# Optimization experiments

Hardware: AMD Instinct MI355X
Metric: run time of the kernel (lower is better)

Reference implementation:

```python
import jax, jax.numpy as jnp
import numpy as np

INPUT_DIM = 16
LW = 128          # layerwidth
NB_LAYERS = 4
NB_X = 4096
NB_THETA = 128
PARAM_COUNT = INPUT_DIM * LW + LW + (NB_LAYERS - 1) * (LW * LW + LW) + LW + 1  # 51841


def setup_inputs() -> dict:
    k1, k2 = jax.random.split(jax.random.key(0))
    x = jax.random.normal(k1, (NB_X, INPUT_DIM), dtype=jnp.float32)
    theta = jax.random.normal(k2, (NB_THETA, PARAM_COUNT), dtype=jnp.float32)
    return {"x": x, "theta": theta}


def reference(x, theta):
    # x: [nb_x, input_dim], theta: [nb_theta, param_count]
    t = theta.shape[0]
    off = 0
    # first layer: W0 [t, LW, INPUT_DIM], b0 [t, LW]
    W0 = theta[:, off:off + INPUT_DIM * LW].reshape(t, LW, INPUT_DIM); off += INPUT_DIM * LW
    b0 = theta[:, off:off + LW]; off += LW
    h = jnp.tanh(jnp.einsum('thi,xi->txh', W0, x) + b0[:, None, :])  # [t, nb_x, LW]
    # hidden layers
    for _ in range(NB_LAYERS - 1):
        W = theta[:, off:off + LW * LW].reshape(t, LW, LW); off += LW * LW
        b = theta[:, off:off + LW]; off += LW
        h = jnp.tanh(jnp.einsum('tho,txo->txh', W, h) + b[:, None, :])
    # output layer: Wl [t, LW], bl [t, 1]
    Wl = theta[:, off:off + LW]; off += LW
    bl = theta[:, off:off + 1]
    out = jnp.einsum('th,txh->tx', Wl, h)[..., None] + bl[:, None, :]  # [t, nb_x, 1]
    return out
```

## Files before the change

kernel.cpp:

```cpp
#include <hip/hip_runtime.h>


#define IND      16
#define LWD      128
#define THREADS  256
#define PARAMS   51841

#define WS_L0    12582912
#define WS_X     (WS_L0 + 128 * 8192)
#define WS_TOTAL (WS_X + 32 * 8192)

#define LDS_B    32768
#define LDS_WL   (32768 + 1536)
#define LDS_SZ   (32768 + 1536 + 520)

typedef _Float16 f16x8 __attribute__((ext_vector_type(8)));
typedef _Float16 f16x4 __attribute__((ext_vector_type(4)));
typedef float    f32x16 __attribute__((ext_vector_type(16)));
typedef float    f32x4v __attribute__((ext_vector_type(4)));
typedef unsigned u32x2  __attribute__((ext_vector_type(2)));

union U4 { unsigned u[4]; f16x8 v; };

__device__ __forceinline__ float fast_tanh(float v) {
    float e = __builtin_amdgcn_exp2f(v * 2.8853900817779268f);
    return 1.0f - 2.0f * __builtin_amdgcn_rcpf(e + 1.0f);
}
__device__ __forceinline__ unsigned pkf16(float a, float b) {
    unsigned short ua = __builtin_bit_cast(unsigned short, (_Float16)a);
    unsigned short ub = __builtin_bit_cast(unsigned short, (_Float16)b);
    return (unsigned)ua | ((unsigned)ub << 16);
}
#define MFMA(A, B, C) __builtin_amdgcn_mfma_f32_32x32x16_f16((A), (B), (C), 0, 0, 0)

__device__ __forceinline__ void gload16(const void* g, void* l) {
    __builtin_amdgcn_global_load_lds(
        (const __attribute__((address_space(1))) void*)g,
        (__attribute__((address_space(3))) void*)l, 16, 0, 0);
}

__device__ __forceinline__ void conv8(const float* __restrict__ s, char* hidst, char* lodst) {
    float v[8];
    *reinterpret_cast<float4*>(v)     = *reinterpret_cast<const float4*>(s);
    *reinterpret_cast<float4*>(v + 4) = *reinterpret_cast<const float4*>(s + 4);
    f16x8 hi, lo;
#pragma unroll
    for (int i = 0; i < 8; ++i) {
        hi[i] = (_Float16)v[i];
        lo[i] = (_Float16)(v[i] - (float)hi[i]);
    }
    *reinterpret_cast<f16x8*>(hidst) = hi;
    *reinterpret_cast<f16x8*>(lodst) = lo;
}

__global__ __launch_bounds__(256)
void prep_kernel(const float* __restrict__ theta, const float* __restrict__ xin,
                 char* __restrict__ ws)
{
    const int b = blockIdx.x, tid = threadIdx.x;
    if (b < 3072) {
        const int t = b / 24, rem = b % 24, li = rem >> 3, hblk = rem & 7;
        const int h  = hblk * 16 + (tid >> 4);
        const int kc = (tid >> 1) & 7, kh = tid & 1;
        const float* src = theta + (size_t)t * PARAMS + 2176 + li * 16512
                         + h * 128 + kc * 16 + kh * 8;
        float v[8];
        *reinterpret_cast<float4*>(v)     = *reinterpret_cast<const float4*>(src);
        *reinterpret_cast<float4*>(v + 4) = *reinterpret_cast<const float4*>(src + 4);
        f16x8 p;
#pragma unroll
        for (int i = 0; i < 8; ++i) p[i] = (_Float16)v[i];
        char* img = ws + ((size_t)(t * 3 + li) << 15);
        *reinterpret_cast<f16x8*>(img + ((h >> 5) * 8 + kc) * 1024
                                      + (kh * 32 + (h & 31)) * 16) = p;
    } else if (b < 3136) {
        const int gid = (b - 3072) * 256 + tid;
        const int t = gid >> 7, h = gid & 127;
        const float* src = theta + (size_t)t * PARAMS + h * IND;
        char* dst = ws + WS_L0 + (size_t)t * 8192 + h * 32;
        conv8(src,     dst,      dst + 4096);
        conv8(src + 8, dst + 16, dst + 4096 + 16);
    } else {
        const int row = (b - 3136) * 256 + tid;
        const float* src = xin + (size_t)row * IND;
        char* dst = ws + WS_X + (size_t)(row >> 7) * 8192 + (row & 127) * 32;
        conv8(src,     dst,      dst + 4096);
        conv8(src + 8, dst + 16, dst + 4096 + 16);
    }
}

__global__ __launch_bounds__(THREADS, 4)
void mlp_main(const float* __restrict__ theta, const char* __restrict__ ws,
              float* __restrict__ out)
{
    __shared__ __align__(16) char sL[LDS_SZ];

    const int tid = threadIdx.x, bid = blockIdx.x;
    const int sw  = (bid & 7) * 512 + (bid >> 3);
    const int t   = sw >> 5, xt = sw & 31;
    const float* __restrict__ th = theta + (size_t)t * PARAMS;
    const int lane = tid & 63, w = tid >> 6, r31 = lane & 31, khalf = lane >> 5;
    const int bpa  = (lane ^ 32) << 2;

    {
        const char* img = ws + ((size_t)(t * 3) << 15);
#pragma unroll
        for (int c = 0; c < 8; ++c)
            gload16(img + (w + c * 4) * 1024 + lane * 16, sL + (w + c * 4) * 1024);
    }
    for (int k = tid; k < 513; k += THREADS) {
        float v = (k < 384) ? th[2176 + (k >> 7) * 16512 + 16384 + (k & 127)]
                            : th[51712 + (k - 384)];
        *reinterpret_cast<float*>(sL + LDS_B + k * 4) = v;
    }

    f32x16 acc[4];
    {
        const char* w0i = ws + WS_L0 + (size_t)t  * 8192;
        const char* xi  = ws + WS_X  + (size_t)xt * 8192;
        const int ro = r31 * 32 + khalf * 16;
        const f16x8 B0h = *reinterpret_cast<const f16x8*>(xi + w * 1024 + ro);
        const f16x8 B0l = *reinterpret_cast<const f16x8*>(xi + 4096 + w * 1024 + ro);
#pragma unroll
        for (int tt = 0; tt < 4; ++tt) {
#pragma unroll
            for (int g = 0; g < 4; ++g) {
                const float4 bv = *reinterpret_cast<const float4*>(
                    th + 2048 + tt * 32 + g * 8 + khalf * 4);
                acc[tt][4 * g + 0] = bv.x; acc[tt][4 * g + 1] = bv.y;
                acc[tt][4 * g + 2] = bv.z; acc[tt][4 * g + 3] = bv.w;
            }
            const f16x8 Ah = *reinterpret_cast<const f16x8*>(w0i + tt * 1024 + ro);
            const f16x8 Al = *reinterpret_cast<const f16x8*>(w0i + 4096 + tt * 1024 + ro);
            acc[tt] = MFMA(Al, B0h, acc[tt]);
            acc[tt] = MFMA(Ah, B0l, acc[tt]);
            acc[tt] = MFMA(Ah, B0h, acc[tt]);
        }
    }

    f16x8 Bf[8];
    auto activate_pack = [&]() {
#pragma unroll
        for (int tt = 0; tt < 4; ++tt) {
            unsigned P0[4], P1[4];
#pragma unroll
            for (int g = 0; g < 4; ++g) {
                const float v0 = fast_tanh(acc[tt][4 * g + 0]);
                const float v1 = fast_tanh(acc[tt][4 * g + 1]);
                const float v2 = fast_tanh(acc[tt][4 * g + 2]);
                const float v3 = fast_tanh(acc[tt][4 * g + 3]);
                P0[g] = pkf16(v0, v1);
                P1[g] = pkf16(v2, v3);
            }
#pragma unroll
            for (int j = 0; j < 2; ++j) {
#if __has_builtin(__builtin_amdgcn_permlane32_swap)
                const u32x2 r0 = __builtin_amdgcn_permlane32_swap(
                    P0[2 * j], P0[2 * j + 1], false, false);
                const u32x2 r1 = __builtin_amdgcn_permlane32_swap(
                    P1[2 * j], P1[2 * j + 1], false, false);
                U4 u;
                u.u[0] = r0[0]; u.u[1] = r1[0]; u.u[2] = r0[1]; u.u[3] = r1[1];
#else
                const unsigned s0 = khalf ? P0[2 * j] : P0[2 * j + 1];
                const unsigned s1 = khalf ? P1[2 * j] : P1[2 * j + 1];
                const unsigned q0 = (unsigned)__builtin_amdgcn_ds_bpermute(bpa, (int)s0);
                const unsigned q1 = (unsigned)__builtin_amdgcn_ds_bpermute(bpa, (int)s1);
                U4 u;
                u.u[0] = khalf ? q0 : P0[2 * j];
                u.u[1] = khalf ? q1 : P1[2 * j];
                u.u[2] = khalf ? P0[2 * j + 1] : q0;
                u.u[3] = khalf ? P1[2 * j + 1] : q1;
#endif
                Bf[2 * tt + j] = u.v;
            }
        }
    };
    activate_pack();
    __syncthreads();

#pragma unroll
    for (int l = 1; l <= 3; ++l) {
        __builtin_amdgcn_s_setprio(1);
#pragma unroll
        for (int tt = 0; tt < 4; ++tt) {
#pragma unroll
            for (int g = 0; g < 4; ++g) {
                const f32x4v bv = *reinterpret_cast<const f32x4v*>(
                    sL + LDS_B + (l - 1) * 512 + (tt * 32 + g * 8) * 4 + khalf * 16);
                acc[tt][4 * g + 0] = bv[0]; acc[tt][4 * g + 1] = bv[1];
                acc[tt][4 * g + 2] = bv[2]; acc[tt][4 * g + 3] = bv[3];
            }
#pragma unroll
            for (int kc = 0; kc < 8; ++kc) {
                const f16x8 a = *reinterpret_cast<const f16x8*>(
                    sL + (tt * 8 + kc) * 1024 + lane * 16);
                acc[tt] = MFMA(a, Bf[kc], acc[tt]);
            }
        }
        __builtin_amdgcn_s_setprio(0);
        if (l < 3) {
            __syncthreads();
            const char* img = ws + ((size_t)(t * 3 + l) << 15);
#pragma unroll
            for (int c = 0; c < 8; ++c)
                gload16(img + (w + c * 4) * 1024 + lane * 16, sL + (w + c * 4) * 1024);
            activate_pack();
            __syncthreads();
        }
    }

    float s = 0.0f;
#pragma unroll
    for (int tt = 0; tt < 4; ++tt)
#pragma unroll
        for (int g = 0; g < 4; ++g) {
            const f32x4v wv = *reinterpret_cast<const f32x4v*>(
                sL + LDS_WL + (tt * 32 + g * 8) * 4 + khalf * 16);
#pragma unroll
            for (int q = 0; q < 4; ++q)
                s = fmaf(fast_tanh(acc[tt][4 * g + q]), wv[q], s);
        }
    const float sp = __builtin_bit_cast(float,
        __builtin_amdgcn_ds_bpermute(bpa, __builtin_bit_cast(int, s)));
    const float res = s + sp + *reinterpret_cast<const float*>(sL + LDS_WL + 512);
    if (!khalf) out[(size_t)t * 4096 + xt * 128 + w * 32 + r31] = res;
}

__global__ __launch_bounds__(THREADS, 1)
void mlp_kernel_fb(const float* __restrict__ xin,
                   const float* __restrict__ theta,
                   float* __restrict__ out)
{
    __shared__ __align__(16) _Float16 sH   [128 * LWD];
    __shared__ __align__(16) _Float16 sWhi [LWD * LWD];
    __shared__ __align__(16) _Float16 sWlo [LWD * LWD];
    __shared__ __align__(16) _Float16 sX0hi[128 * IND];
    __shared__ __align__(16) _Float16 sX0lo[128 * IND];
    __shared__ __align__(16) _Float16 sW0hi[LWD * IND];
    __shared__ __align__(16) _Float16 sW0lo[LWD * IND];
    __shared__ float sB[2][LWD];
    __shared__ float sWl[LWD + 1];

    const int tid = threadIdx.x;
    const int bid = blockIdx.x;
    const int sw  = (bid & 7) * 512 + (bid >> 3);
    const int t   = sw >> 5;
    const int xt  = sw & 31;
    const float* __restrict__ th = theta + (size_t)t * PARAMS;
    const float* __restrict__ xg = xin   + (size_t)xt * (128 * IND);

#pragma unroll
    for (int j = 0; j < 2; ++j) {
        const int flat = j * 1024 + tid * 4;
        const float4 v = *reinterpret_cast<const float4*>(xg + flat);
        _Float16 h0 = (_Float16)v.x, h1 = (_Float16)v.y, h2 = (_Float16)v.z, h3 = (_Float16)v.w;
        f16x4 ph = {h0, h1, h2, h3};
        f16x4 pl = {(_Float16)(v.x - (float)h0), (_Float16)(v.y - (float)h1),
                    (_Float16)(v.z - (float)h2), (_Float16)(v.w - (float)h3)};
        *reinterpret_cast<f16x4*>(&sX0hi[flat]) = ph;
        *reinterpret_cast<f16x4*>(&sX0lo[flat]) = pl;
    }
#pragma unroll
    for (int j = 0; j < 2; ++j) {
        const int flat = j * 1024 + tid * 4;
        const float a0 = th[flat], a1 = th[flat + 1], a2 = th[flat + 2], a3 = th[flat + 3];
        _Float16 h0 = (_Float16)a0, h1 = (_Float16)a1, h2 = (_Float16)a2, h3 = (_Float16)a3;
        f16x4 ph = {h0, h1, h2, h3};
        f16x4 pl = {(_Float16)(a0 - (float)h0), (_Float16)(a1 - (float)h1),
                    (_Float16)(a2 - (float)h2), (_Float16)(a3 - (float)h3)};
        *reinterpret_cast<f16x4*>(&sW0hi[flat]) = ph;
        *reinterpret_cast<f16x4*>(&sW0lo[flat]) = pl;
    }
    if (tid < LWD) sB[0][tid] = th[IND * LWD + tid];
    __syncthreads();

    const int lane  = tid & 63;
    const int w     = tid >> 6;
    const int r31   = lane & 31;
    const int khalf = lane >> 5;
    const int hb    = (w >> 1) * 64;
    const int xb    = (w & 1) * 64;
    const int hA0 = hb + r31,  hA1 = hb + 32 + r31;
    const int xB0 = xb + r31,  xB1 = xb + 32 + r31;
    const int swzA0 = (hA0 & 15) << 4, swzA1 = (hA1 & 15) << 4;
    const int swzB0 = (xB0 & 15) << 4, swzB1 = (xB1 & 15) << 4;

    f32x16 acc[2][2];

    {
        const int kb = khalf * 16;
        f16x8 ah[2], al[2], bh[2], bl[2];
        ah[0] = *reinterpret_cast<const f16x8*>((const char*)sW0hi + hA0 * 32 + kb);
        ah[1] = *reinterpret_cast<const f16x8*>((const char*)sW0hi + hA1 * 32 + kb);
        al[0] = *reinterpret_cast<const f16x8*>((const char*)sW0lo + hA0 * 32 + kb);
        al[1] = *reinterpret_cast<const f16x8*>((const char*)sW0lo + hA1 * 32 + kb);
        bh[0] = *reinterpret_cast<const f16x8*>((const char*)sX0hi + xB0 * 32 + kb);
        bh[1] = *reinterpret_cast<const f16x8*>((const char*)sX0hi + xB1 * 32 + kb);
        bl[0] = *reinterpret_cast<const f16x8*>((const char*)sX0lo + xB0 * 32 + kb);
        bl[1] = *reinterpret_cast<const f16x8*>((const char*)sX0lo + xB1 * 32 + kb);
#pragma unroll
        for (int tt = 0; tt < 2; ++tt)
#pragma unroll
            for (int tx = 0; tx < 2; ++tx) {
                f32x16 a;
#pragma unroll
                for (int i = 0; i < 16; ++i) a[i] = 0.0f;
                a = MFMA(al[tt], bh[tx], a);
                a = MFMA(ah[tt], bl[tx], a);
                a = MFMA(ah[tt], bh[tx], a);
                acc[tt][tx] = a;
            }
    }

    auto epilogue = [&](const float* __restrict__ bb) {
#pragma unroll
        for (int tt = 0; tt < 2; ++tt)
#pragma unroll
            for (int tx = 0; tx < 2; ++tx) {
                const int xw  = xb + tx * 32 + r31;
                const int swz = (xw & 15) << 4;
#pragma unroll
                for (int g = 0; g < 4; ++g) {
                    const int hbase = hb + tt * 32 + g * 8 + khalf * 4;
                    f16x4 pk;
#pragma unroll
                    for (int q = 0; q < 4; ++q) {
                        const float v = acc[tt][tx][g * 4 + q] + bb[hbase + q];
                        pk[q] = (_Float16)(1.0f - 2.0f * __builtin_amdgcn_rcpf(
                            __builtin_amdgcn_exp2f(v * 2.8853900817779268f) + 1.0f));
                    }
                    *reinterpret_cast<f16x4*>((char*)sH + xw * 256 + ((hbase * 2) ^ swz)) = pk;
                }
            }
    };

    for (int l = 0; l < 3; ++l) {
        __syncthreads();
        const float* __restrict__ wsrc = th + 2176 + l * 16512;
#pragma unroll
        for (int j = 0; j < 16; ++j) {
            const int flat = j * 1024 + tid * 4;
            const int hrow = flat >> 7;
            const int o    = flat & 127;
            const float a0 = wsrc[flat], a1 = wsrc[flat + 1], a2 = wsrc[flat + 2], a3 = wsrc[flat + 3];
            _Float16 h0 = (_Float16)a0, h1 = (_Float16)a1, h2 = (_Float16)a2, h3 = (_Float16)a3;
            f16x4 ph = {h0, h1, h2, h3};
            f16x4 pl = {(_Float16)(a0 - (float)h0), (_Float16)(a1 - (float)h1),
                        (_Float16)(a2 - (float)h2), (_Float16)(a3 - (float)h3)};
            const int boff = hrow * 256 + ((o * 2) ^ ((hrow & 15) << 4));
            *reinterpret_cast<f16x4*>((char*)sWhi + boff) = ph;
            *reinterpret_cast<f16x4*>((char*)sWlo + boff) = pl;
        }
        if (tid < LWD) sB[(l + 1) & 1][tid] = wsrc[LWD * LWD + tid];
        if (l == 2) {
            if (tid < LWD) sWl[tid] = th[51712 + tid];
            if (tid == LWD) sWl[LWD] = th[51840];
        }

        epilogue(sB[l & 1]);
        __syncthreads();

#pragma unroll
        for (int tt = 0; tt < 2; ++tt)
#pragma unroll
            for (int tx = 0; tx < 2; ++tx)
#pragma unroll
                for (int i = 0; i < 16; ++i) acc[tt][tx][i] = 0.0f;
#pragma unroll
        for (int kc = 0; kc < 8; ++kc) {
            const int kb = kc * 32 + khalf * 16;
            f16x8 ah[2], al[2], bv[2];
            ah[0] = *reinterpret_cast<const f16x8*>((const char*)sWhi + hA0 * 256 + (kb ^ swzA0));
            ah[1] = *reinterpret_cast<const f16x8*>((const char*)sWhi + hA1 * 256 + (kb ^ swzA1));
            al[0] = *reinterpret_cast<const f16x8*>((const char*)sWlo + hA0 * 256 + (kb ^ swzA0));
            al[1] = *reinterpret_cast<const f16x8*>((const char*)sWlo + hA1 * 256 + (kb ^ swzA1));
            bv[0] = *reinterpret_cast<const f16x8*>((const char*)sH   + xB0 * 256 + (kb ^ swzB0));
            bv[1] = *reinterpret_cast<const f16x8*>((const char*)sH   + xB1 * 256 + (kb ^ swzB1));
#pragma unroll
            for (int tt = 0; tt < 2; ++tt)
#pragma unroll
                for (int tx = 0; tx < 2; ++tx) {
                    acc[tt][tx] = MFMA(al[tt], bv[tx], acc[tt][tx]);
                    acc[tt][tx] = MFMA(ah[tt], bv[tx], acc[tt][tx]);
                }
        }
    }

    __syncthreads();
    epilogue(sB[1]);
    __syncthreads();

    if (tid < 128) {
        const int r   = tid;
        const int swz = (r & 15) << 4;
        float s = 0.0f;
#pragma unroll
        for (int c = 0; c < 16; ++c) {
            const int hc = (c + r) & 15;
            const f16x8 hv = *reinterpret_cast<const f16x8*>(
                (const char*)sH + r * 256 + ((hc * 16) ^ swz));
#pragma unroll
            for (int q = 0; q < 8; ++q) s += (float)hv[q] * sWl[hc * 8 + q];
        }
        out[(size_t)t * 4096 + (size_t)xt * 128 + r] = s + sWl[LWD];
    }
}

extern "C" void kernel_launch(void* const* d_in, const int* in_sizes, int n_in,
                              void* d_out, int out_size, void* d_ws, size_t ws_size,
                              hipStream_t stream)
{
    const float* x     = (const float*)d_in[0];
    const float* theta = (const float*)d_in[1];
    float* out = (float*)d_out;

    if (ws_size >= (size_t)WS_TOTAL) {
        prep_kernel<<<dim3(3152), dim3(256), 0, stream>>>(theta, x, (char*)d_ws);
        mlp_main<<<dim3(4096), dim3(THREADS), 0, stream>>>(theta, (const char*)d_ws, out);
    } else {
        mlp_kernel_fb<<<dim3(4096), dim3(THREADS), 0, stream>>>(x, theta, out);
    }
}
```

Baseline: 105.2 us.

## Fold biases and output layer into MFMA via ones-column trick

```diff
diff --git a/kernel.cpp b/kernel.cpp
--- a/kernel.cpp
+++ b/kernel.cpp
@@ -6,22 +6,28 @@
 #define THREADS  256
 #define PARAMS   51841
 
-#define WS_L0    12582912
-#define WS_X     (WS_L0 + 128 * 8192)
-#define WS_TOTAL (WS_X + 32 * 8192)
-
-#define LDS_B    32768
-#define LDS_WL   (32768 + 1536)
-#define LDS_SZ   (32768 + 1536 + 520)
+#define HID_STRIDE 36864
+#define WS_W0    (128 * 3 * HID_STRIDE)
+#define WS_XI    (WS_W0 + 128 * 16384)
+#define WS_TOTAL (WS_XI + 32 * 8192)
+
+#define LDS_WL   36864
+#define LDS_BL   37376
+#define LDS_SZ   37380
 
 typedef _Float16 f16x8 __attribute__((ext_vector_type(8)));
 typedef _Float16 f16x4 __attribute__((ext_vector_type(4)));
 typedef float    f32x16 __attribute__((ext_vector_type(16)));
-typedef float    f32x4v __attribute__((ext_vector_type(4)));
 typedef unsigned u32x2  __attribute__((ext_vector_type(2)));
 
 union U4 { unsigned u[4]; f16x8 v; };
 
+__device__ __forceinline__ f32x16 zero16() {
+    f32x16 z;
+#pragma unroll
+    for (int i = 0; i < 16; ++i) z[i] = 0.0f;
+    return z;
+}
 __device__ __forceinline__ float fast_tanh(float v) {
     float e = __builtin_amdgcn_exp2f(v * 2.8853900817779268f);
     return 1.0f - 2.0f * __builtin_amdgcn_rcpf(e + 1.0f);
@@ -70,20 +76,58 @@
         f16x8 p;
 #pragma unroll
         for (int i = 0; i < 8; ++i) p[i] = (_Float16)v[i];
-        char* img = ws + ((size_t)(t * 3 + li) << 15);
-        *reinterpret_cast<f16x8*>(img + ((h >> 5) * 8 + kc) * 1024
+        char* img = ws + (size_t)(t * 3 + li) * HID_STRIDE;
+        *reinterpret_cast<f16x8*>(img + ((h >> 5) * 9 + kc) * 1024
                                       + (kh * 32 + (h & 31)) * 16) = p;
-    } else if (b < 3136) {
-        const int gid = (b - 3072) * 256 + tid;
+    } else if (b < 3456) {
+        const int idx = b - 3072, t = idx / 3, li = idx % 3;
+        const int tt = tid >> 6, l6 = tid & 63, kh = l6 >> 5, row = l6 & 31;
+        f16x8 p;
+#pragma unroll
+        for (int i = 0; i < 8; ++i) p[i] = (_Float16)0.0f;
+        if (kh == 0) {
+            const float bv = theta[(size_t)t * PARAMS + 2176 + li * 16512
+                                   + 16384 + tt * 32 + row];
+            p[0] = (_Float16)bv;
+            p[1] = (_Float16)(bv - (float)p[0]);
+        }
+        char* img = ws + (size_t)(t * 3 + li) * HID_STRIDE;
+        *reinterpret_cast<f16x8*>(img + (tt * 9 + 8) * 1024 + l6 * 16) = p;
+    } else if (b < 3520) {
+        const int gid = (b - 3456) * 256 + tid;
         const int t = gid >> 7, h = gid & 127;
         const float* src = theta + (size_t)t * PARAMS + h * IND;
-        char* dst = ws + WS_L0 + (size_t)t * 8192 + h * 32;
+        char* dst = ws + WS_W0 + (size_t)t * 16384 + h * 32;
         conv8(src,     dst,      dst + 4096);
         conv8(src + 8, dst + 16, dst + 4096 + 16);
+    } else if (b < 3648) {
+        const int t = b - 3520;
+        const float* th = theta + (size_t)t * PARAMS;
+        char* base = ws + WS_W0 + (size_t)t * 16384;
+        {
+            const int tt = tid >> 6, l6 = tid & 63, kh = l6 >> 5, row = l6 & 31;
+            f16x8 p;
+#pragma unroll
+            for (int i = 0; i < 8; ++i) p[i] = (_Float16)0.0f;
+            if (kh == 0) {
+                const float bv = th[2048 + tt * 32 + row];
+                p[0] = (_Float16)bv;
+                p[1] = (_Float16)(bv - (float)p[0]);
+            }
+            *reinterpret_cast<f16x8*>(base + 8192 + tt * 1024 + l6 * 16) = p;
+        }
+        if (tid < 32) {
+            const int kc = tid >> 1, kh = tid & 1;
+            const float* src = th + 51712 + kc * 16 + kh * 8;
+            f16x8 p;
+#pragma unroll
+            for (int i = 0; i < 8; ++i) p[i] = (_Float16)src[i];
+            *reinterpret_cast<f16x8*>(base + 12288 + tid * 16) = p;
+        }
     } else {
-        const int row = (b - 3136) * 256 + tid;
+        const int row = (b - 3648) * 256 + tid;
         const float* src = xin + (size_t)row * IND;
-        char* dst = ws + WS_X + (size_t)(row >> 7) * 8192 + (row & 127) * 32;
+        char* dst = ws + WS_XI + (size_t)(row >> 7) * 8192 + (row & 127) * 32;
         conv8(src,     dst,      dst + 4096);
         conv8(src + 8, dst + 16, dst + 4096 + 16);
     }
@@ -101,40 +145,42 @@
     const float* __restrict__ th = theta + (size_t)t * PARAMS;
     const int lane = tid & 63, w = tid >> 6, r31 = lane & 31, khalf = lane >> 5;
     const int bpa  = (lane ^ 32) << 2;
+    (void)bpa;
+
+    U4 ubias;
+    ubias.u[0] = khalf ? 0u : 0x3C003C00u;
+    ubias.u[1] = 0u; ubias.u[2] = 0u; ubias.u[3] = 0u;
+    const f16x8 Bones = ubias.v;
 
     {
-        const char* img = ws + ((size_t)(t * 3) << 15);
-#pragma unroll
-        for (int c = 0; c < 8; ++c)
-            gload16(img + (w + c * 4) * 1024 + lane * 16, sL + (w + c * 4) * 1024);
-    }
-    for (int k = tid; k < 513; k += THREADS) {
-        float v = (k < 384) ? th[2176 + (k >> 7) * 16512 + 16384 + (k & 127)]
-                            : th[51712 + (k - 384)];
-        *reinterpret_cast<float*>(sL + LDS_B + k * 4) = v;
+        const char* img = ws + (size_t)(t * 3) * HID_STRIDE;
+#pragma unroll
+        for (int c = 0; c < 9; ++c)
+            gload16(img + (c * 4 + w) * 1024 + lane * 16, sL + (c * 4 + w) * 1024);
+        if (tid < 32)
+            gload16(ws + WS_W0 + (size_t)t * 16384 + 12288 + tid * 16,
+                    sL + LDS_WL + tid * 16);
+        if (tid == 32) *reinterpret_cast<float*>(sL + LDS_BL) = th[51840];
     }
 
     f32x16 acc[4];
     {
-        const char* w0i = ws + WS_L0 + (size_t)t  * 8192;
-        const char* xi  = ws + WS_X  + (size_t)xt * 8192;
+        const char* w0i = ws + WS_W0 + (size_t)t  * 16384;
+        const char* xi  = ws + WS_XI + (size_t)xt * 8192;
         const int ro = r31 * 32 + khalf * 16;
         const f16x8 B0h = *reinterpret_cast<const f16x8*>(xi + w * 1024 + ro);
         const f16x8 B0l = *reinterpret_cast<const f16x8*>(xi + 4096 + w * 1024 + ro);
 #pragma unroll
         for (int tt = 0; tt < 4; ++tt) {
-#pragma unroll
-            for (int g = 0; g < 4; ++g) {
-                const float4 bv = *reinterpret_cast<const float4*>(
-                    th + 2048 + tt * 32 + g * 8 + khalf * 4);
-                acc[tt][4 * g + 0] = bv.x; acc[tt][4 * g + 1] = bv.y;
-                acc[tt][4 * g + 2] = bv.z; acc[tt][4 * g + 3] = bv.w;
-            }
+            f32x16 a = zero16();
+            const f16x8 Ab = *reinterpret_cast<const f16x8*>(w0i + 8192 + tt * 1024 + lane * 16);
+            a = MFMA(Ab, Bones, a);
             const f16x8 Ah = *reinterpret_cast<const f16x8*>(w0i + tt * 1024 + ro);
             const f16x8 Al = *reinterpret_cast<const f16x8*>(w0i + 4096 + tt * 1024 + ro);
-            acc[tt] = MFMA(Al, B0h, acc[tt]);
-            acc[tt] = MFMA(Ah, B0l, acc[tt]);
-            acc[tt] = MFMA(Ah, B0h, acc[tt]);
+            a = MFMA(Al, B0h, a);
+            a = MFMA(Ah, B0l, a);
+            a = MFMA(Ah, B0h, a);
+            acc[tt] = a;
         }
     }
 
@@ -184,47 +230,39 @@
         __builtin_amdgcn_s_setprio(1);
 #pragma unroll
         for (int tt = 0; tt < 4; ++tt) {
-#pragma unroll
-            for (int g = 0; g < 4; ++g) {
-                const f32x4v bv = *reinterpret_cast<const f32x4v*>(
-                    sL + LDS_B + (l - 1) * 512 + (tt * 32 + g * 8) * 4 + khalf * 16);
-                acc[tt][4 * g + 0] = bv[0]; acc[tt][4 * g + 1] = bv[1];
-                acc[tt][4 * g + 2] = bv[2]; acc[tt][4 * g + 3] = bv[3];
-            }
+            f32x16 a = zero16();
+            a = MFMA(*reinterpret_cast<const f16x8*>(
+                         sL + (tt * 9 + 8) * 1024 + lane * 16), Bones, a);
 #pragma unroll
             for (int kc = 0; kc < 8; ++kc) {
-                const f16x8 a = *reinterpret_cast<const f16x8*>(
-                    sL + (tt * 8 + kc) * 1024 + lane * 16);
-                acc[tt] = MFMA(a, Bf[kc], acc[tt]);
-            }
+                const f16x8 av = *reinterpret_cast<const f16x8*>(
+                    sL + (tt * 9 + kc) * 1024 + lane * 16);
+                a = MFMA(av, Bf[kc], a);
+            }
+            acc[tt] = a;
         }
         __builtin_amdgcn_s_setprio(0);
         if (l < 3) {
             __syncthreads();
-            const char* img = ws + ((size_t)(t * 3 + l) << 15);
-#pragma unroll
-            for (int c = 0; c < 8; ++c)
-                gload16(img + (w + c * 4) * 1024 + lane * 16, sL + (w + c * 4) * 1024);
+            const char* img = ws + (size_t)(t * 3 + l) * HID_STRIDE;
+#pragma unroll
+            for (int c = 0; c < 9; ++c)
+                gload16(img + (c * 4 + w) * 1024 + lane * 16, sL + (c * 4 + w) * 1024);
             activate_pack();
             __syncthreads();
         }
     }
 
-    float s = 0.0f;
-#pragma unroll
-    for (int tt = 0; tt < 4; ++tt)
-#pragma unroll
-        for (int g = 0; g < 4; ++g) {
-            const f32x4v wv = *reinterpret_cast<const f32x4v*>(
-                sL + LDS_WL + (tt * 32 + g * 8) * 4 + khalf * 16);
-#pragma unroll
-            for (int q = 0; q < 4; ++q)
-                s = fmaf(fast_tanh(acc[tt][4 * g + q]), wv[q], s);
-        }
-    const float sp = __builtin_bit_cast(float,
-        __builtin_amdgcn_ds_bpermute(bpa, __builtin_bit_cast(int, s)));
-    const float res = s + sp + *reinterpret_cast<const float*>(sL + LDS_WL + 512);
-    if (!khalf) out[(size_t)t * 4096 + xt * 128 + w * 32 + r31] = res;
+    activate_pack();
+    const float bl = *reinterpret_cast<const float*>(sL + LDS_BL);
+    f32x16 af = zero16();
+#pragma unroll
+    for (int kc = 0; kc < 8; ++kc) {
+        const f16x8 wv = *reinterpret_cast<const f16x8*>(
+            sL + LDS_WL + (kc * 2 + khalf) * 16);
+        af = MFMA(wv, Bf[kc], af);
+    }
+    if (!khalf) out[(size_t)t * 4096 + xt * 128 + w * 32 + r31] = af[0] + bl;
 }
 
 __global__ __launch_bounds__(THREADS, 1)
@@ -416,7 +454,7 @@
     float* out = (float*)d_out;
 
     if (ws_size >= (size_t)WS_TOTAL) {
-        prep_kernel<<<dim3(3152), dim3(256), 0, stream>>>(theta, x, (char*)d_ws);
+        prep_kernel<<<dim3(3664), dim3(256), 0, stream>>>(theta, x, (char*)d_ws);
         mlp_main<<<dim3(4096), dim3(THREADS), 0, stream>>>(theta, (const char*)d_ws, out);
     } else {
         mlp_kernel_fb<<<dim3(4096), dim3(THREADS), 0, stream>>>(x, theta, out);
```

Result: slower. 109.6 us (+4.2%).

## Drop LDS staging, prescale weights by tanh constant, read weights directly from global

Applied to the files above, without the earlier changes.

```diff
diff --git a/kernel.cpp b/kernel.cpp
--- a/kernel.cpp
+++ b/kernel.cpp
@@ -2,17 +2,15 @@
 
 
 #define IND      16
-#define LWD      128
 #define THREADS  256
 #define PARAMS   51841
-
-#define WS_L0    12582912
-#define WS_X     (WS_L0 + 128 * 8192)
-#define WS_TOTAL (WS_X + 32 * 8192)
-
-#define LDS_B    32768
-#define LDS_WL   (32768 + 1536)
-#define LDS_SZ   (32768 + 1536 + 520)
+#define SCALE    2.8853900817779268f
+
+#define HID_STRIDE 32768
+#define WS_T     (128 * 3 * HID_STRIDE)
+#define T_STRIDE 16384
+#define WS_XI    (WS_T + 128 * T_STRIDE)
+#define WS_TOTAL (WS_XI + 32 * 8192)
 
 typedef _Float16 f16x8 __attribute__((ext_vector_type(8)));
 typedef _Float16 f16x4 __attribute__((ext_vector_type(4)));
@@ -22,32 +20,34 @@
 
 union U4 { unsigned u[4]; f16x8 v; };
 
-__device__ __forceinline__ float fast_tanh(float v) {
-    float e = __builtin_amdgcn_exp2f(v * 2.8853900817779268f);
-    return 1.0f - 2.0f * __builtin_amdgcn_rcpf(e + 1.0f);
-}
-__device__ __forceinline__ unsigned pkf16(float a, float b) {
-    unsigned short ua = __builtin_bit_cast(unsigned short, (_Float16)a);
-    unsigned short ub = __builtin_bit_cast(unsigned short, (_Float16)b);
-    return (unsigned)ua | ((unsigned)ub << 16);
-}
+__device__ __forceinline__ unsigned tanh2pk(float z0, float z1) {
+    const float t0 = __builtin_amdgcn_exp2f(-__builtin_fabsf(z0));
+    const float t1 = __builtin_amdgcn_exp2f(-__builtin_fabsf(z1));
+    const float d0 = t0 + 1.0f, d1 = t1 + 1.0f;
+    float r0 = __builtin_fmaf(d0, __builtin_fmaf(d0, 0.32302f, -1.45380f), 2.12094f);
+    float r1 = __builtin_fmaf(d1, __builtin_fmaf(d1, 0.32302f, -1.45380f), 2.12094f);
+    r0 = __builtin_fmaf(r0, __builtin_fmaf(-d0, r0, 1.0f), r0);
+    r1 = __builtin_fmaf(r1, __builtin_fmaf(-d1, r1, 1.0f), r1);
+    const float u0 = __builtin_fmaf(t0 * r0, -2.0f, 1.0f);
+    const float u1 = __builtin_fmaf(t1 * r1, -2.0f, 1.0f);
+    const float y0 = __builtin_copysignf(u0, z0);
+    const float y1 = __builtin_copysignf(u1, z1);
+    return __builtin_bit_cast(unsigned, __builtin_amdgcn_cvt_pkrtz(y0, y1));
+}
+
 #define MFMA(A, B, C) __builtin_amdgcn_mfma_f32_32x32x16_f16((A), (B), (C), 0, 0, 0)
 
-__device__ __forceinline__ void gload16(const void* g, void* l) {
-    __builtin_amdgcn_global_load_lds(
-        (const __attribute__((address_space(1))) void*)g,
-        (__attribute__((address_space(3))) void*)l, 16, 0, 0);
-}
-
-__device__ __forceinline__ void conv8(const float* __restrict__ s, char* hidst, char* lodst) {
+__device__ __forceinline__ void conv8(const float* __restrict__ s, char* hidst,
+                                      char* lodst, float scale) {
     float v[8];
     *reinterpret_cast<float4*>(v)     = *reinterpret_cast<const float4*>(s);
     *reinterpret_cast<float4*>(v + 4) = *reinterpret_cast<const float4*>(s + 4);
     f16x8 hi, lo;
 #pragma unroll
     for (int i = 0; i < 8; ++i) {
-        hi[i] = (_Float16)v[i];
-        lo[i] = (_Float16)(v[i] - (float)hi[i]);
+        const float sv = v[i] * scale;
+        hi[i] = (_Float16)sv;
+        lo[i] = (_Float16)(sv - (float)hi[i]);
     }
     *reinterpret_cast<f16x8*>(hidst) = hi;
     *reinterpret_cast<f16x8*>(lodst) = lo;
@@ -69,55 +69,56 @@
         *reinterpret_cast<float4*>(v + 4) = *reinterpret_cast<const float4*>(src + 4);
         f16x8 p;
 #pragma unroll
-        for (int i = 0; i < 8; ++i) p[i] = (_Float16)v[i];
-        char* img = ws + ((size_t)(t * 3 + li) << 15);
+        for (int i = 0; i < 8; ++i) p[i] = (_Float16)(v[i] * SCALE);
+        char* img = ws + (size_t)(t * 3 + li) * HID_STRIDE;
         *reinterpret_cast<f16x8*>(img + ((h >> 5) * 8 + kc) * 1024
                                       + (kh * 32 + (h & 31)) * 16) = p;
     } else if (b < 3136) {
         const int gid = (b - 3072) * 256 + tid;
         const int t = gid >> 7, h = gid & 127;
         const float* src = theta + (size_t)t * PARAMS + h * IND;
-        char* dst = ws + WS_L0 + (size_t)t * 8192 + h * 32;
-        conv8(src,     dst,      dst + 4096);
-        conv8(src + 8, dst + 16, dst + 4096 + 16);
+        char* dst = ws + WS_T + (size_t)t * T_STRIDE + h * 32;
+        conv8(src,     dst,      dst + 4096,      SCALE);
+        conv8(src + 8, dst + 16, dst + 4096 + 16, SCALE);
+    } else if (b < 3264) {
+        const int t = b - 3136;
+        const float* th = theta + (size_t)t * PARAMS;
+        char* base = ws + WS_T + (size_t)t * T_STRIDE;
+        if (tid < 128)
+            *reinterpret_cast<float*>(base + 8192 + tid * 4) = SCALE * th[2048 + tid];
+        for (int k = tid; k < 384; k += 256)
+            *reinterpret_cast<float*>(base + 8704 + k * 4) =
+                SCALE * th[2176 + (k >> 7) * 16512 + 16384 + (k & 127)];
+        if (tid < 128)
+            *reinterpret_cast<float*>(base + 10240 + tid * 4) = th[51712 + tid];
+        if (tid == 0)
+            *reinterpret_cast<float*>(base + 10752) = th[51840];
     } else {
-        const int row = (b - 3136) * 256 + tid;
+        const int row = (b - 3264) * 256 + tid;
         const float* src = xin + (size_t)row * IND;
-        char* dst = ws + WS_X + (size_t)(row >> 7) * 8192 + (row & 127) * 32;
-        conv8(src,     dst,      dst + 4096);
-        conv8(src + 8, dst + 16, dst + 4096 + 16);
-    }
-}
-
-__global__ __launch_bounds__(THREADS, 4)
-void mlp_main(const float* __restrict__ theta, const char* __restrict__ ws,
-              float* __restrict__ out)
+        char* dst = ws + WS_XI + (size_t)(row >> 7) * 8192 + (row & 127) * 32;
+        conv8(src,     dst,      dst + 4096,      1.0f);
+        conv8(src + 8, dst + 16, dst + 4096 + 16, 1.0f);
+    }
+}
+
+__global__ __launch_bounds__(THREADS, 3)
+void mlp_main(const char* __restrict__ ws, float* __restrict__ out)
 {
-    __shared__ __align__(16) char sL[LDS_SZ];
-
     const int tid = threadIdx.x, bid = blockIdx.x;
     const int sw  = (bid & 7) * 512 + (bid >> 3);
     const int t   = sw >> 5, xt = sw & 31;
-    const float* __restrict__ th = theta + (size_t)t * PARAMS;
     const int lane = tid & 63, w = tid >> 6, r31 = lane & 31, khalf = lane >> 5;
     const int bpa  = (lane ^ 32) << 2;
+    (void)bpa;
+
+    const char* wt = ws + WS_T + (size_t)t * T_STRIDE;
+
+    f32x16 acc[4];
+    f16x8  Bf[8];
 
     {
-        const char* img = ws + ((size_t)(t * 3) << 15);
-#pragma unroll
-        for (int c = 0; c < 8; ++c)
-            gload16(img + (w + c * 4) * 1024 + lane * 16, sL + (w + c * 4) * 1024);
-    }
-    for (int k = tid; k < 513; k += THREADS) {
-        float v = (k < 384) ? th[2176 + (k >> 7) * 16512 + 16384 + (k & 127)]
-                            : th[51712 + (k - 384)];
-        *reinterpret_cast<float*>(sL + LDS_B + k * 4) = v;
-    }
-
-    f32x16 acc[4];
-    {
-        const char* w0i = ws + WS_L0 + (size_t)t  * 8192;
-        const char* xi  = ws + WS_X  + (size_t)xt * 8192;
+        const char* xi = ws + WS_XI + (size_t)xt * 8192;
         const int ro = r31 * 32 + khalf * 16;
         const f16x8 B0h = *reinterpret_cast<const f16x8*>(xi + w * 1024 + ro);
         const f16x8 B0l = *reinterpret_cast<const f16x8*>(xi + 4096 + w * 1024 + ro);
@@ -125,32 +126,27 @@
         for (int tt = 0; tt < 4; ++tt) {
 #pragma unroll
             for (int g = 0; g < 4; ++g) {
-                const float4 bv = *reinterpret_cast<const float4*>(
-                    th + 2048 + tt * 32 + g * 8 + khalf * 4);
-                acc[tt][4 * g + 0] = bv.x; acc[tt][4 * g + 1] = bv.y;
-                acc[tt][4 * g + 2] = bv.z; acc[tt][4 * g + 3] = bv.w;
-            }
-            const f16x8 Ah = *reinterpret_cast<const f16x8*>(w0i + tt * 1024 + ro);
-            const f16x8 Al = *reinterpret_cast<const f16x8*>(w0i + 4096 + tt * 1024 + ro);
+                const f32x4v bv = *reinterpret_cast<const f32x4v*>(
+                    wt + 8192 + (tt * 32 + g * 8 + khalf * 4) * 4);
+                acc[tt][4 * g + 0] = bv[0]; acc[tt][4 * g + 1] = bv[1];
+                acc[tt][4 * g + 2] = bv[2]; acc[tt][4 * g + 3] = bv[3];
+            }
+            const f16x8 Ah = *reinterpret_cast<const f16x8*>(wt + tt * 1024 + ro);
+            const f16x8 Al = *reinterpret_cast<const f16x8*>(wt + 4096 + tt * 1024 + ro);
             acc[tt] = MFMA(Al, B0h, acc[tt]);
             acc[tt] = MFMA(Ah, B0l, acc[tt]);
             acc[tt] = MFMA(Ah, B0h, acc[tt]);
         }
     }
 
-    f16x8 Bf[8];
     auto activate_pack = [&]() {
 #pragma unroll
         for (int tt = 0; tt < 4; ++tt) {
             unsigned P0[4], P1[4];
 #pragma unroll
             for (int g = 0; g < 4; ++g) {
-                const float v0 = fast_tanh(acc[tt][4 * g + 0]);
-                const float v1 = fast_tanh(acc[tt][4 * g + 1]);
-                const float v2 = fast_tanh(acc[tt][4 * g + 2]);
-                const float v3 = fast_tanh(acc[tt][4 * g + 3]);
-                P0[g] = pkf16(v0, v1);
-                P1[g] = pkf16(v2, v3);
+                P0[g] = tanh2pk(acc[tt][4 * g + 0], acc[tt][4 * g + 1]);
+                P1[g] = tanh2pk(acc[tt][4 * g + 2], acc[tt][4 * g + 3]);
             }
 #pragma unroll
             for (int j = 0; j < 2; ++j) {
@@ -177,53 +173,68 @@
         }
     };
     activate_pack();
-    __syncthreads();
-
-#pragma unroll
-    for (int l = 1; l <= 3; ++l) {
-        __builtin_amdgcn_s_setprio(1);
+
+#pragma unroll
+    for (int l = 0; l < 3; ++l) {
+        const char* img  = ws + (size_t)(t * 3 + l) * HID_STRIDE;
+        const char* bias = wt + 8704 + l * 512;
 #pragma unroll
         for (int tt = 0; tt < 4; ++tt) {
 #pragma unroll
             for (int g = 0; g < 4; ++g) {
                 const f32x4v bv = *reinterpret_cast<const f32x4v*>(
-                    sL + LDS_B + (l - 1) * 512 + (tt * 32 + g * 8) * 4 + khalf * 16);
+                    bias + (tt * 32 + g * 8 + khalf * 4) * 4);
                 acc[tt][4 * g + 0] = bv[0]; acc[tt][4 * g + 1] = bv[1];
                 acc[tt][4 * g + 2] = bv[2]; acc[tt][4 * g + 3] = bv[3];
             }
-#pragma unroll
-            for (int kc = 0; kc < 8; ++kc) {
-                const f16x8 a = *reinterpret_cast<const f16x8*>(
-                    sL + (tt * 8 + kc) * 1024 + lane * 16);
-                acc[tt] = MFMA(a, Bf[kc], acc[tt]);
-            }
-        }
-        __builtin_amdgcn_s_setprio(0);
-        if (l < 3) {
-            __syncthreads();
-            const char* img = ws + ((size_t)(t * 3 + l) << 15);
-#pragma unroll
-            for (int c = 0; c < 8; ++c)
-                gload16(img + (w + c * 4) * 1024 + lane * 16, sL + (w + c * 4) * 1024);
-            activate_pack();
-            __syncthreads();
-        }
+        }
+#pragma unroll
+        for (int kc = 0; kc < 8; ++kc)
+#pragma unroll
+            for (int tt = 0; tt < 4; ++tt) {
+                const f16x8 av = *reinterpret_cast<const f16x8*>(
+                    img + (tt * 8 + kc) * 1024 + lane * 16);
+                acc[tt] = MFMA(av, Bf[kc], acc[tt]);
+            }
+        activate_pack();
     }
 
     float s = 0.0f;
 #pragma unroll
-    for (int tt = 0; tt < 4; ++tt)
-#pragma unroll
-        for (int g = 0; g < 4; ++g) {
-            const f32x4v wv = *reinterpret_cast<const f32x4v*>(
-                sL + LDS_WL + (tt * 32 + g * 8) * 4 + khalf * 16);
-#pragma unroll
-            for (int q = 0; q < 4; ++q)
-                s = fmaf(fast_tanh(acc[tt][4 * g + q]), wv[q], s);
-        }
+    for (int kc = 0; kc < 8; ++kc) {
+        (void)kc;
+    }
+    {
+        const char* wl = wt + 10240;
+#pragma unroll
+        for (int tt = 0; tt < 4; ++tt)
+#pragma unroll
+            for (int g = 0; g < 4; ++g) {
+                const f32x4v wv = *reinterpret_cast<const f32x4v*>(
+                    wl + (tt * 32 + g * 8 + khalf * 4) * 4);
+                const float z0 = acc[tt][4 * g + 0], z1 = acc[tt][4 * g + 1];
+                const float z2 = acc[tt][4 * g + 2], z3 = acc[tt][4 * g + 3];
+                const float e0 = __builtin_amdgcn_exp2f(-__builtin_fabsf(z0));
+                const float e1 = __builtin_amdgcn_exp2f(-__builtin_fabsf(z1));
+                const float e2 = __builtin_amdgcn_exp2f(-__builtin_fabsf(z2));
+                const float e3 = __builtin_amdgcn_exp2f(-__builtin_fabsf(z3));
+                const float y0 = __builtin_copysignf(
+                    __builtin_fmaf(e0 * __builtin_amdgcn_rcpf(1.0f + e0), -2.0f, 1.0f), z0);
+                const float y1 = __builtin_copysignf(
+                    __builtin_fmaf(e1 * __builtin_amdgcn_rcpf(1.0f + e1), -2.0f, 1.0f), z1);
+                const float y2 = __builtin_copysignf(
+                    __builtin_fmaf(e2 * __builtin_amdgcn_rcpf(1.0f + e2), -2.0f, 1.0f), z2);
+                const float y3 = __builtin_copysignf(
+                    __builtin_fmaf(e3 * __builtin_amdgcn_rcpf(1.0f + e3), -2.0f, 1.0f), z3);
+                s = __builtin_fmaf(y0, wv[0], s);
+                s = __builtin_fmaf(y1, wv[1], s);
+                s = __builtin_fmaf(y2, wv[2], s);
+                s = __builtin_fmaf(y3, wv[3], s);
+            }
+    }
     const float sp = __builtin_bit_cast(float,
         __builtin_amdgcn_ds_bpermute(bpa, __builtin_bit_cast(int, s)));
-    const float res = s + sp + *reinterpret_cast<const float*>(sL + LDS_WL + 512);
+    const float res = s + sp + *reinterpret_cast<const float*>(wt + 10752);
     if (!khalf) out[(size_t)t * 4096 + xt * 128 + w * 32 + r31] = res;
 }
 
@@ -232,15 +243,15 @@
                    const float* __restrict__ theta,
                    float* __restrict__ out)
 {
-    __shared__ __align__(16) _Float16 sH   [128 * LWD];
-    __shared__ __align__(16) _Float16 sWhi [LWD * LWD];
-    __shared__ __align__(16) _Float16 sWlo [LWD * LWD];
+    __shared__ __align__(16) _Float16 sH   [128 * 128];
+    __shared__ __align__(16) _Float16 sWhi [128 * 128];
+    __shared__ __align__(16) _Float16 sWlo [128 * 128];
     __shared__ __align__(16) _Float16 sX0hi[128 * IND];
     __shared__ __align__(16) _Float16 sX0lo[128 * IND];
-    __shared__ __align__(16) _Float16 sW0hi[LWD * IND];
-    __shared__ __align__(16) _Float16 sW0lo[LWD * IND];
-    __shared__ float sB[2][LWD];
-    __shared__ float sWl[LWD + 1];
+    __shared__ __align__(16) _Float16 sW0hi[128 * IND];
+    __shared__ __align__(16) _Float16 sW0lo[128 * IND];
+    __shared__ float sB[2][128];
+    __shared__ float sWl[129];
 
     const int tid = threadIdx.x;
     const int bid = blockIdx.x;
@@ -272,7 +283,7 @@
         *reinterpret_cast<f16x4*>(&sW0hi[flat]) = ph;
         *reinterpret_cast<f16x4*>(&sW0lo[flat]) = pl;
     }
-    if (tid < LWD) sB[0][tid] = th[IND * LWD + tid];
+    if (tid < 128) sB[0][tid] = th[IND * 128 + tid];
     __syncthreads();
 
     const int lane  = tid & 63;
@@ -352,10 +363,10 @@
             *reinterpret_cast<f16x4*>((char*)sWhi + boff) = ph;
             *reinterpret_cast<f16x4*>((char*)sWlo + boff) = pl;
         }
-        if (tid < LWD) sB[(l + 1) & 1][tid] = wsrc[LWD * LWD + tid];
+        if (tid < 128) sB[(l + 1) & 1][tid] = wsrc[128 * 128 + tid];
         if (l == 2) {
-            if (tid < LWD) sWl[tid] = th[51712 + tid];
-            if (tid == LWD) sWl[LWD] = th[51840];
+            if (tid < 128) sWl[tid] = th[51712 + tid];
+            if (tid == 128) sWl[128] = th[51840];
         }
 
         epilogue(sB[l & 1]);
@@ -403,7 +414,7 @@
 #pragma unroll
             for (int q = 0; q < 8; ++q) s += (float)hv[q] * sWl[hc * 8 + q];
         }
-        out[(size_t)t * 4096 + (size_t)xt * 128 + r] = s + sWl[LWD];
+        out[(size_t)t * 4096 + (size_t)xt * 128 + r] = s + sWl[128];
     }
 }
 
@@ -416,8 +427,8 @@
     float* out = (float*)d_out;
 
     if (ws_size >= (size_t)WS_TOTAL) {
-        prep_kernel<<<dim3(3152), dim3(256), 0, stream>>>(theta, x, (char*)d_ws);
-        mlp_main<<<dim3(4096), dim3(THREADS), 0, stream>>>(theta, (const char*)d_ws, out);
+        prep_kernel<<<dim3(3280), dim3(256), 0, stream>>>(theta, x, (char*)d_ws);
+        mlp_main<<<dim3(4096), dim3(THREADS), 0, stream>>>((const char*)d_ws, out);
     } else {
         mlp_kernel_fb<<<dim3(4096), dim3(THREADS), 0, stream>>>(x, theta, out);
     }
```

Measured after the change: 187.2 us. 78.0% more time.
